# Performance work log

Measured on AMD Instinct MI355X. Metric: run time of the kernel, lower is better.

Reference implementation:

```python
import jax, jax.numpy as jnp
import numpy as np

N_NODES = 50000
N_EDGES = 800000
MUL = 32      # node feature multiplicity (32x0e)
A = 8         # node attr multiplicity (8x0e)
VE = 4        # edge attr multiplicity (4x0e)
FC_IN = 16    # edge_scalars dim (fc_neurons[0])
FC_H = 64     # fc hidden (fc_neurons[1])
W_NUMEL = MUL * VE  # tp.weight_numel for 'uvu' instruction = 128
NUM_NEIGHBORS = 16
N_LAYERS = 2


def fctp(x, y, w):
    # FullyConnectedTensorProduct on pure scalars: x[n,U], y[n,V], w[U,V,K]
    U, V = w.shape[0], w.shape[1]
    return jnp.einsum('nu,nv,uvk->nk', x, y, w) / np.float32(np.sqrt(U * V))


def tp_uvu(x, y, w):
    # 'uvu' TensorProduct with per-edge weights: x[e,U], y[e,V], w[e,U,V]
    V = y.shape[1]
    return jnp.einsum('eu,ev,euv->eu', x, y, w) / np.float32(np.sqrt(V))


def conv_layer(node_in, node_attr, edge_src, edge_dst, edge_attr, edge_scalars,
               sc_w, lin1_w, lin2_w, alpha_w, sce_w, fc_w0, fc_w1):
    n_nodes = node_in.shape[0]
    # per-edge weight generation (FullyConnectedNet with sin activation)
    h = jnp.sin(edge_scalars @ fc_w0 / np.float32(np.sqrt(FC_IN)))          # [E, FC_H]
    w = (h @ fc_w1 / np.float32(np.sqrt(FC_H))).reshape(-1, MUL, VE)        # [E, MUL, VE]
    # self connection + lin1
    node_sc = fctp(node_in, node_attr, sc_w)                                # [N, K]
    x = fctp(node_in, node_attr, lin1_w)                                    # [N, MUL]
    # gather -> tensor product -> scatter-add
    edge_features = tp_uvu(x[edge_src], edge_attr, w)                       # [E, MUL]
    node_features = jax.ops.segment_sum(edge_features, edge_dst,
                                        num_segments=n_nodes)
    node_features = node_features / np.float32(np.sqrt(NUM_NEIGHBORS))      # [N, MUL]
    node_conv = fctp(node_features, node_attr, lin2_w)                      # [N, K]
    alpha = fctp(node_features, node_attr, alpha_w)                         # [N, 1]
    # output_mask is all ones for scalar outputs -> alpha = 1 - 1 + alpha*1
    node_out = node_sc + alpha * node_conv
    edge_out = edge_attr + fctp(edge_features, edge_attr, sce_w) / np.float32(np.sqrt(NUM_NEIGHBORS))
    return node_out, edge_out


def setup_inputs() -> dict:
    key = jax.random.key(0)
    ks = jax.random.split(key, 13)
    L = N_LAYERS
    return {
        'node_features': jax.random.normal(ks[0], (N_NODES, MUL), jnp.float32),
        'node_attr':     jax.random.normal(ks[1], (N_NODES, A), jnp.float32),
        'edge_src':      jax.random.randint(ks[2], (N_EDGES,), 0, N_NODES),
        'edge_dst':      jax.random.randint(ks[3], (N_EDGES,), 0, N_NODES),
        'edge_attr':     jax.random.normal(ks[4], (N_EDGES, VE), jnp.float32),
        'edge_scalars':  jax.random.normal(ks[5], (N_EDGES, FC_IN), jnp.float32),
        # stacked per-layer parameters
        'sc_w':    jax.random.normal(ks[6],  (L, MUL, A, MUL), jnp.float32),
        'lin1_w':  jax.random.normal(ks[7],  (L, MUL, A, MUL), jnp.float32),
        'lin2_w':  jax.random.normal(ks[8],  (L, MUL, A, MUL), jnp.float32),
        'alpha_w': 0.1 * jax.random.normal(ks[9], (L, MUL, A, 1), jnp.float32),
        'sce_w':   jax.random.normal(ks[10], (L, MUL, VE, VE), jnp.float32),
        'fc_w0':   jax.random.normal(ks[11], (L, FC_IN, FC_H), jnp.float32),
        'fc_w1':   jax.random.normal(ks[12], (L, FC_H, W_NUMEL), jnp.float32),
    }


def reference(node_features, node_attr, edge_src, edge_dst, edge_attr, edge_scalars,
              sc_w, lin1_w, lin2_w, alpha_w, sce_w, fc_w0, fc_w1):
    nf, ea = node_features, edge_attr
    for l in range(N_LAYERS):
        nf, ea = conv_layer(nf, node_attr, edge_src, edge_dst, ea, edge_scalars,
                            sc_w[l], lin1_w[l], lin2_w[l], alpha_w[l],
                            sce_w[l], fc_w0[l], fc_w1[l])
        if l < N_LAYERS - 1:
            nf = jnp.sin(nf)  # Gate over even scalars == elementwise sin
    return nf, ea
```

## Files before the change

kernel.cpp:

```cpp
#include <hip/hip_runtime.h>
#include <hip/hip_bf16.h>


namespace {
constexpr int NN = 50000;
constexpr int NE = 800000;
constexpr int SCAN_BLOCKS = 196;

constexpr long OFF_NF   = 0;
constexpr long OFF_W0P  = 1600000;
constexpr long OFF_W2P  = 1602048;
constexpr long OFF_WNP  = 1610240;
constexpr long OFF_OFF  = 1638912;
constexpr long OFF_CUR  = 1688913;
constexpr long OFF_PERM = 1738913;
constexpr long OFF_BSUM = 2538913;
constexpr long OFF_EF   = 2539172;
}

typedef __attribute__((ext_vector_type(8))) short short8;
typedef __attribute__((ext_vector_type(4))) float f32x4;
typedef unsigned int   __attribute__((may_alias)) u32a;
typedef unsigned short __attribute__((may_alias)) u16a;
typedef float          __attribute__((may_alias)) f32a;

__device__ __forceinline__ float us2f(unsigned int u) {
    unsigned int x = u << 16; float f;
    __builtin_memcpy(&f, &x, sizeof(f));
    return f;
}
__device__ __forceinline__ unsigned short f2us(float f) {
    __hip_bfloat16 h = __float2bfloat16(f);
    unsigned short s;
    __builtin_memcpy(&s, &h, sizeof(s));
    return s;
}

__global__ __launch_bounds__(256) void k_hist(
        const int* __restrict__ dst, int* __restrict__ cnt,
        const float* __restrict__ f0, const float* __restrict__ f1,
        const float* __restrict__ l1w, const float* __restrict__ scw,
        const float* __restrict__ l2w, const float* __restrict__ aw,
        unsigned short* __restrict__ w0p, unsigned short* __restrict__ w2p,
        unsigned short* __restrict__ wnp) {
    int i = blockIdx.x * 256 + threadIdx.x;
    if (i < NE) atomicAdd(&cnt[dst[i]], 1);
    if (i < 4096) {
        int l = i >> 11, r = i & 2047;
        int nt = r >> 9, lane = (r >> 3) & 63, ii = r & 7;
        int k = (lane >> 4) * 8 + ii;
        int j = nt * 16 + (lane & 15);
        float v = (k < 16) ? 0.25f * f0[l * 1024 + k * 64 + j] : 0.f;
        w0p[i] = f2us(v);
    }
    if (i < 16384) {
        int l = i >> 13, r = i & 8191;
        int g = r >> 9;
        int kt = g >> 1, nt = g & 1;
        int lane = (r >> 3) & 63, ii = r & 7;
        int K = kt * 32 + (lane >> 4) * 8 + ii;
        int j = K >> 2, v = K & 3;
        int u = nt * 16 + (lane & 15);
        w2p[i] = f2us(f1[l * 8192 + j * 128 + u * 4 + v]);
    }
    if (i < 57344) {
        int l = i / 28672, r = i % 28672;
        int tile = r >> 12;
        int r2 = r & 4095;
        int kt = r2 >> 9, lane = (r2 >> 3) & 63, ii = r2 & 7;
        int k = kt * 32 + (lane >> 4) * 8 + ii;
        int u = k >> 3, v = k & 7;
        int col = lane & 15;
        int uvb = l * 8192 + (u * 8 + v) * 32;
        float val;
        if (tile < 2)      val = l1w[uvb + tile * 16 + col];
        else if (tile < 4) val = scw[uvb + (tile - 2) * 16 + col];
        else if (tile < 6) val = l2w[uvb + (tile - 4) * 16 + col];
        else               val = (col == 0) ? aw[l * 256 + u * 8 + v] : 0.f;
        wnp[i] = f2us(val);
    }
}

__global__ __launch_bounds__(256) void k_scan1(const int* __restrict__ cnt,
                                               int* __restrict__ bsum) {
    __shared__ int s[256];
    int t = threadIdx.x;
    int i = blockIdx.x * 256 + t;
    s[t] = (i < NN) ? cnt[i] : 0;
    __syncthreads();
    for (int d = 128; d > 0; d >>= 1) {
        if (t < d) s[t] += s[t + d];
        __syncthreads();
    }
    if (t == 0) bsum[blockIdx.x] = s[0];
}

__global__ __launch_bounds__(256) void k_scan2(int* __restrict__ bsum) {
    __shared__ int s[256];
    int t = threadIdx.x;
    int v = (t < SCAN_BLOCKS) ? bsum[t] : 0;
    s[t] = v; __syncthreads();
    for (int d = 1; d < 256; d <<= 1) {
        int x = (t >= d) ? s[t - d] : 0;
        __syncthreads();
        s[t] += x;
        __syncthreads();
    }
    if (t < SCAN_BLOCKS) bsum[t] = s[t] - v;
}

__global__ __launch_bounds__(256) void k_scan3(
        const int* __restrict__ cnt, const int* __restrict__ bsum,
        int* __restrict__ off, int* __restrict__ cur) {
    __shared__ int s[256];
    int t = threadIdx.x;
    int i = blockIdx.x * 256 + t;
    int v = (i < NN) ? cnt[i] : 0;
    s[t] = v; __syncthreads();
    for (int d = 1; d < 256; d <<= 1) {
        int x = (t >= d) ? s[t - d] : 0;
        __syncthreads();
        s[t] += x;
        __syncthreads();
    }
    int excl = s[t] - v + bsum[blockIdx.x];
    if (i < NN) { off[i] = excl; cur[i] = excl; }
    if (i == NN - 1) off[NN] = excl + v;
}

__global__ void k_perm(const int* __restrict__ dst, int* __restrict__ cur,
                       int* __restrict__ perm) {
    int e = blockIdx.x * 256 + threadIdx.x;
    if (e >= NE) return;
    perm[e] = atomicAdd(&cur[dst[e]], 1);
}

__device__ __forceinline__ void stage_xy(const float* __restrict__ nf,
                                         const float* __restrict__ nattr,
                                         long n0, int t, f32a* Xs, f32a* Ys) {
    {
        long e = n0 * 32 + t * 8;
        int n = t >> 2, u = (t & 3) * 8;
        f32a* d = &Xs[n * 33 + u];
        if (e + 8 <= (long)NN * 32) {
            const float4* p = (const float4*)(nf + e);
            float4 q0 = p[0], q1 = p[1];
            d[0]=q0.x; d[1]=q0.y; d[2]=q0.z; d[3]=q0.w;
            d[4]=q1.x; d[5]=q1.y; d[6]=q1.z; d[7]=q1.w;
        } else {
#pragma unroll
            for (int i = 0; i < 8; i++)
                d[i] = (e + i < (long)NN * 32) ? nf[e + i] : 0.f;
        }
    }
    if (t < 128) {
        long e = n0 * 8 + t * 4;
        int n = t >> 1, v = (t & 1) * 4;
        f32a* d = &Ys[n * 9 + v];
        if (e + 4 <= (long)NN * 8) {
            float4 q = *(const float4*)(nattr + e);
            d[0]=q.x; d[1]=q.y; d[2]=q.z; d[3]=q.w;
        } else {
#pragma unroll
            for (int i = 0; i < 4; i++)
                d[i] = (e + i < (long)NN * 8) ? nattr[e + i] : 0.f;
        }
    }
}

__global__ __launch_bounds__(256) void k_npre_m(
        const float* __restrict__ nf, const float* __restrict__ nattr,
        const unsigned short* __restrict__ wnp_l, float* __restrict__ xl) {
    __shared__ f32a Xs[64 * 33];
    __shared__ f32a Ys[64 * 9];
    const int t = threadIdx.x;
    const long n0 = (long)blockIdx.x * 64;
    stage_xy(nf, nattr, n0, t, Xs, Ys);
    __syncthreads();

    const int lane = t & 63, w = t >> 6;
    const int l15 = lane & 15, quad = lane >> 4;
    const int nb = w * 16;
    float y[8], xk[8];
#pragma unroll
    for (int v = 0; v < 8; v++) y[v] = Ys[(nb + l15) * 9 + v];
#pragma unroll
    for (int kt = 0; kt < 8; kt++) xk[kt] = Xs[(nb + l15) * 33 + kt * 4 + quad];

    f32x4 a0, a1;
    a0[0]=0.f;a0[1]=0.f;a0[2]=0.f;a0[3]=0.f;
    a1[0]=0.f;a1[1]=0.f;a1[2]=0.f;a1[3]=0.f;
#pragma unroll
    for (int kt = 0; kt < 8; kt++) {
        float xv = xk[kt];
        short8 a;
#pragma unroll
        for (int i = 0; i < 8; i++) a[i] = (short)f2us(xv * y[i]);
        const short8 b0 = *(const short8*)(wnp_l + ((0 * 8 + kt) * 512) + lane * 8);
        const short8 b1 = *(const short8*)(wnp_l + ((1 * 8 + kt) * 512) + lane * 8);
        a0 = __builtin_amdgcn_mfma_f32_16x16x32_bf16(a, b0, a0, 0, 0, 0);
        a1 = __builtin_amdgcn_mfma_f32_16x16x32_bf16(a, b1, a1, 0, 0, 0);
    }
#pragma unroll
    for (int r = 0; r < 4; r++) {
        long n = n0 + nb + quad * 4 + r;
        if (n < NN) {
            xl[n * 32 + l15]      = a0[r] * 0.0625f;
            xl[n * 32 + 16 + l15] = a1[r] * 0.0625f;
        }
    }
}

__global__ __launch_bounds__(256) void k_edge_w(
        const float* __restrict__ esc, const int* __restrict__ srcp,
        const int* __restrict__ perm, const float* __restrict__ ea_in,
        float* __restrict__ ea_out, const float* __restrict__ xl,
        const unsigned short* __restrict__ w0p,
        const unsigned short* __restrict__ w2p,
        const float* __restrict__ sew, unsigned short* __restrict__ ef_bf) {
    __shared__ __align__(16) unsigned char SCR[4][8704];

    const int t = threadIdx.x;
    const int w = t >> 6, lane = t & 63;
    const int l15 = lane & 15, quad = lane >> 4;
    const long e0 = ((long)blockIdx.x * 4 + w) * 64;
    u16a* Hs = (u16a*)SCR[w];
    f32a* Ts = (f32a*)SCR[w];

    short8 bw0[4];
#pragma unroll
    for (int nt = 0; nt < 4; nt++)
        bw0[nt] = *(const short8*)(w0p + (nt * 64 + lane) * 8);
#pragma unroll
    for (int mt = 0; mt < 4; mt++) {
        int row = mt * 16 + l15;
        short8 a;
#pragma unroll
        for (int i = 0; i < 8; i++) a[i] = 0;
        if (quad < 2) {
            const float4* ep = (const float4*)(esc + (e0 + row) * 16 + quad * 8);
            float4 p0 = ep[0], p1 = ep[1];
            a[0]=(short)f2us(p0.x); a[1]=(short)f2us(p0.y);
            a[2]=(short)f2us(p0.z); a[3]=(short)f2us(p0.w);
            a[4]=(short)f2us(p1.x); a[5]=(short)f2us(p1.y);
            a[6]=(short)f2us(p1.z); a[7]=(short)f2us(p1.w);
        }
#pragma unroll
        for (int nt = 0; nt < 4; nt++) {
            f32x4 c; c[0]=0.f; c[1]=0.f; c[2]=0.f; c[3]=0.f;
            c = __builtin_amdgcn_mfma_f32_16x16x32_bf16(a, bw0[nt], c, 0, 0, 0);
#pragma unroll
            for (int r = 0; r < 4; r++) {
                int edge = mt * 16 + quad * 4 + r;
                int j = nt * 16 + l15;
                Hs[edge * 68 + j] = f2us(__sinf(c[r]));
            }
        }
    }
    __syncthreads();

    f32x4 acc[4][2];
#pragma unroll
    for (int mt = 0; mt < 4; mt++)
#pragma unroll
        for (int nt = 0; nt < 2; nt++) {
            acc[mt][nt][0]=0.f; acc[mt][nt][1]=0.f;
            acc[mt][nt][2]=0.f; acc[mt][nt][3]=0.f;
        }
#pragma unroll
    for (int mt = 0; mt < 4; mt++) {
        int row = mt * 16 + l15;
        float4 eaq = ((const float4*)ea_in)[e0 + row];
#pragma unroll
        for (int kt = 0; kt < 8; kt++) {
            unsigned int hp = *(const u32a*)(Hs + row * 68 + kt * 8 + quad * 2);
            float H0 = us2f(hp & 0xFFFFu), H1 = us2f(hp >> 16);
            short8 a;
            a[0]=(short)f2us(H0*eaq.x); a[1]=(short)f2us(H0*eaq.y);
            a[2]=(short)f2us(H0*eaq.z); a[3]=(short)f2us(H0*eaq.w);
            a[4]=(short)f2us(H1*eaq.x); a[5]=(short)f2us(H1*eaq.y);
            a[6]=(short)f2us(H1*eaq.z); a[7]=(short)f2us(H1*eaq.w);
            const short8 b0 = *(const short8*)(w2p + ((kt*2+0)*64 + lane) * 8);
            const short8 b1 = *(const short8*)(w2p + ((kt*2+1)*64 + lane) * 8);
            acc[mt][0] = __builtin_amdgcn_mfma_f32_16x16x32_bf16(a, b0, acc[mt][0], 0, 0, 0);
            acc[mt][1] = __builtin_amdgcn_mfma_f32_16x16x32_bf16(a, b1, acc[mt][1], 0, 0, 0);
        }
    }
    __syncthreads();
#pragma unroll
    for (int mt = 0; mt < 4; mt++)
#pragma unroll
        for (int nt = 0; nt < 2; nt++)
#pragma unroll
            for (int r = 0; r < 4; r++)
                Ts[(mt*16 + quad*4 + r) * 34 + nt*16 + l15] = acc[mt][nt][r] * 0.125f;

    {
        long ge = e0 + lane;
        float tv[32];
#pragma unroll
        for (int u = 0; u < 32; u++) tv[u] = Ts[lane * 34 + u];
        int src = srcp[ge], pm = perm[ge];
        float4 eaq = ((const float4*)ea_in)[ge];
        float ea[4] = {eaq.x, eaq.y, eaq.z, eaq.w};
        const float4* xp = (const float4*)(xl + (long)src * 32);
        float ef[32];
#pragma unroll
        for (int g = 0; g < 8; g++) {
            float4 xq = xp[g];
            ef[4*g+0] = 0.5f * xq.x * tv[4*g+0];
            ef[4*g+1] = 0.5f * xq.y * tv[4*g+1];
            ef[4*g+2] = 0.5f * xq.z * tv[4*g+2];
            ef[4*g+3] = 0.5f * xq.w * tv[4*g+3];
        }
        uint4* efp = (uint4*)(ef_bf + (long)pm * 32);
#pragma unroll
        for (int g = 0; g < 4; g++) {
            uint4 wv;
            wv.x = (unsigned)f2us(ef[8*g+0]) | ((unsigned)f2us(ef[8*g+1]) << 16);
            wv.y = (unsigned)f2us(ef[8*g+2]) | ((unsigned)f2us(ef[8*g+3]) << 16);
            wv.z = (unsigned)f2us(ef[8*g+4]) | ((unsigned)f2us(ef[8*g+5]) << 16);
            wv.w = (unsigned)f2us(ef[8*g+6]) | ((unsigned)f2us(ef[8*g+7]) << 16);
            efp[g] = wv;
        }
        float eo[4] = {0.f, 0.f, 0.f, 0.f};
#pragma unroll
        for (int u = 0; u < 32; u++) {
            float efu = ef[u];
#pragma unroll
            for (int v = 0; v < 4; v++) {
                float p = efu * ea[v];
                const float* sw = sew + (u * 4 + v) * 4;
#pragma unroll
                for (int k = 0; k < 4; k++) eo[k] = fmaf(p, sw[k], eo[k]);
            }
        }
        constexpr float SCE_SCALE = 0.02209708691f;
        float4 o;
        o.x = ea[0] + eo[0]*SCE_SCALE; o.y = ea[1] + eo[1]*SCE_SCALE;
        o.z = ea[2] + eo[2]*SCE_SCALE; o.w = ea[3] + eo[3]*SCE_SCALE;
        ((float4*)ea_out)[ge] = o;
    }
}

__global__ __launch_bounds__(256) void k_gpost_m(
        const int* __restrict__ off, const unsigned short* __restrict__ ef,
        const float* __restrict__ nf_cur, const float* __restrict__ nattr,
        const unsigned short* __restrict__ wnp_l,
        float* __restrict__ nf_next, float* __restrict__ out_nf, int last) {
    __shared__ f32a Xs[64 * 33];
    __shared__ f32a As[64 * 33];
    __shared__ f32a Ys[64 * 9];
    const int t = threadIdx.x;
    const long n0 = (long)blockIdx.x * 64;
    stage_xy(nf_cur, nattr, n0, t, Xs, Ys);

    {
        int slot = t >> 3, g = (t >> 2) & 1, l4 = t & 3;
#pragma unroll
        for (int batch = 0; batch < 2; batch++) {
            int nl = batch * 32 + slot;
            long n = n0 + nl;
            float v[8] = {0.f,0.f,0.f,0.f,0.f,0.f,0.f,0.f};
            if (n < NN) {
                int b = off[n] + g, en = off[n + 1];
                for (int r = b; r < en; r += 2) {
                    uint4 q = *(const uint4*)(ef + (long)r * 32 + l4 * 8);
                    v[0] += us2f(q.x & 0xFFFFu); v[1] += us2f(q.x >> 16);
                    v[2] += us2f(q.y & 0xFFFFu); v[3] += us2f(q.y >> 16);
                    v[4] += us2f(q.z & 0xFFFFu); v[5] += us2f(q.z >> 16);
                    v[6] += us2f(q.w & 0xFFFFu); v[7] += us2f(q.w >> 16);
                }
            }
#pragma unroll
            for (int i = 0; i < 8; i++) v[i] += __shfl_xor(v[i], 4);
            if (g == 0) {
#pragma unroll
                for (int i = 0; i < 8; i++)
                    As[nl * 33 + l4 * 8 + i] = v[i] * 0.25f;
            }
        }
    }
    __syncthreads();

    const int lane = t & 63, w = t >> 6;
    const int l15 = lane & 15, quad = lane >> 4;
    const int nb = w * 16;
    float y[8], xk[8], ak[8];
#pragma unroll
    for (int v = 0; v < 8; v++) y[v] = Ys[(nb + l15) * 9 + v];
#pragma unroll
    for (int kt = 0; kt < 8; kt++) {
        xk[kt] = Xs[(nb + l15) * 33 + kt * 4 + quad];
        ak[kt] = As[(nb + l15) * 33 + kt * 4 + quad];
    }
    f32x4 sc0, sc1, l20, l21, al;
    sc0[0]=0.f;sc0[1]=0.f;sc0[2]=0.f;sc0[3]=0.f;
    sc1 = sc0; l20 = sc0; l21 = sc0; al = sc0;
#pragma unroll
    for (int kt = 0; kt < 8; kt++) {
        float xv = xk[kt], av = ak[kt];
        short8 ax, ag;
#pragma unroll
        for (int i = 0; i < 8; i++) {
            ax[i] = (short)f2us(xv * y[i]);
            ag[i] = (short)f2us(av * y[i]);
        }
        const short8 b2 = *(const short8*)(wnp_l + ((2 * 8 + kt) * 512) + lane * 8);
        const short8 b3 = *(const short8*)(wnp_l + ((3 * 8 + kt) * 512) + lane * 8);
        const short8 b4 = *(const short8*)(wnp_l + ((4 * 8 + kt) * 512) + lane * 8);
        const short8 b5 = *(const short8*)(wnp_l + ((5 * 8 + kt) * 512) + lane * 8);
        const short8 b6 = *(const short8*)(wnp_l + ((6 * 8 + kt) * 512) + lane * 8);
        sc0 = __builtin_amdgcn_mfma_f32_16x16x32_bf16(ax, b2, sc0, 0, 0, 0);
        sc1 = __builtin_amdgcn_mfma_f32_16x16x32_bf16(ax, b3, sc1, 0, 0, 0);
        l20 = __builtin_amdgcn_mfma_f32_16x16x32_bf16(ag, b4, l20, 0, 0, 0);
        l21 = __builtin_amdgcn_mfma_f32_16x16x32_bf16(ag, b5, l21, 0, 0, 0);
        al  = __builtin_amdgcn_mfma_f32_16x16x32_bf16(ag, b6, al,  0, 0, 0);
    }
#pragma unroll
    for (int r = 0; r < 4; r++) {
        float alpha = __shfl(al[r], quad * 16) * 0.0625f;
        long n = n0 + nb + quad * 4 + r;
        if (n < NN) {
            float o0 = sc0[r] * 0.0625f + alpha * (l20[r] * 0.0625f);
            float o1 = sc1[r] * 0.0625f + alpha * (l21[r] * 0.0625f);
            if (last) {
                out_nf[n * 32 + l15]      = o0;
                out_nf[n * 32 + 16 + l15] = o1;
            } else {
                nf_next[n * 32 + l15]      = __sinf(o0);
                nf_next[n * 32 + 16 + l15] = __sinf(o1);
            }
        }
    }
}

extern "C" void kernel_launch(void* const* d_in, const int* in_sizes, int n_in,
                              void* d_out, int out_size, void* d_ws, size_t ws_size,
                              hipStream_t stream) {
    int I_nf, I_na, I_esrc, I_edst, I_ea, I_esc, I_sc, I_l1, I_l2, I_al, I_se, I_f0, I_f1;
    if (in_sizes[0] == 1600000) {
        I_nf=0; I_na=1; I_esrc=2; I_edst=3; I_ea=4; I_esc=5;
        I_sc=6; I_l1=7; I_l2=8; I_al=9; I_se=10; I_f0=11; I_f1=12;
    } else {
        I_al=0; I_ea=1; I_edst=2; I_esc=3; I_esrc=4; I_f0=5; I_f1=6;
        I_l1=7; I_l2=8; I_na=9; I_nf=10; I_sc=11; I_se=12;
    }
    const float* nf_in = (const float*)d_in[I_nf];
    const float* na    = (const float*)d_in[I_na];
    const int*   esrc  = (const int*)d_in[I_esrc];
    const int*   edst  = (const int*)d_in[I_edst];
    const float* ea_in = (const float*)d_in[I_ea];
    const float* escl  = (const float*)d_in[I_esc];
    const float* w_sc  = (const float*)d_in[I_sc];
    const float* w_l1  = (const float*)d_in[I_l1];
    const float* w_l2  = (const float*)d_in[I_l2];
    const float* w_al  = (const float*)d_in[I_al];
    const float* w_se  = (const float*)d_in[I_se];
    const float* w_f0  = (const float*)d_in[I_f0];
    const float* w_f1  = (const float*)d_in[I_f1];

    float* ws = (float*)d_ws;
    float* out_nf = (float*)d_out;
    float* out_ea = out_nf + (long)NN * 32;

    unsigned short* w0p     = (unsigned short*)(ws + OFF_W0P);
    unsigned short* w2p     = (unsigned short*)(ws + OFF_W2P);
    unsigned short* wnp     = (unsigned short*)(ws + OFF_WNP);
    int*            csr_off = (int*)(ws + OFF_OFF);
    int*            csr_cur = (int*)(ws + OFF_CUR);
    int*            perm    = (int*)(ws + OFF_PERM);
    int*            bsum    = (int*)(ws + OFF_BSUM);
    unsigned short* ef_bf   = (unsigned short*)(ws + OFF_EF);

    hipMemsetAsync(csr_cur, 0, NN * sizeof(int), stream);
    k_hist<<<3125, 256, 0, stream>>>(edst, csr_cur, w_f0, w_f1,
                                     w_l1, w_sc, w_l2, w_al, w0p, w2p, wnp);
    k_scan1<<<SCAN_BLOCKS, 256, 0, stream>>>(csr_cur, bsum);
    k_scan2<<<1, 256, 0, stream>>>(bsum);
    k_scan3<<<SCAN_BLOCKS, 256, 0, stream>>>(csr_cur, bsum, csr_off, csr_cur);
    k_perm<<<3125, 256, 0, stream>>>(edst, csr_cur, perm);

    for (int l = 0; l < 2; l++) {
        int last = (l == 1);
        const float* nf_cur = (l == 0) ? nf_in : (ws + OFF_NF);
        const float* ea_cur = (l == 0) ? ea_in : out_ea;

        k_npre_m<<<782, 256, 0, stream>>>(nf_cur, na, wnp + l * 28672,
                                          out_nf );
        k_edge_w<<<3125, 256, 0, stream>>>(escl, esrc, perm, ea_cur, out_ea,
                                           out_nf , w0p + l * 2048,
                                           w2p + l * 8192, w_se + l * 512,
                                           ef_bf);
        k_gpost_m<<<782, 256, 0, stream>>>(csr_off, ef_bf,
                                           nf_cur, na, wnp + l * 28672,
                                           ws + OFF_NF, out_nf, last);
    }
}
```

Baseline: 406.6 us.

## Fuse next-layer lin1 into gather-post kernel and use packed bf16 conversions

Merges the second layer's node pre-transform (lin1) into the first layer's gather/post kernel, so the sin-activated node features are reused from shared memory instead of being re-read by a separate launch. It also replaces scalar float-to-bf16 conversions with a packed two-value conversion builtin where available. The edge weight GEMM loop is reordered so B fragments are loaded once per k-step across all row tiles. The extra kernel phase adds synchronisation and register pressure in the post kernel.

```diff
diff --git a/kernel.cpp b/kernel.cpp
--- a/kernel.cpp
+++ b/kernel.cpp
@@ -34,6 +34,27 @@
     unsigned short s;
     __builtin_memcpy(&s, &h, sizeof(s));
     return s;
+}
+
+#if defined(__has_builtin)
+#  if __has_builtin(__builtin_amdgcn_cvt_pk_bf16_f32)
+#    define PKBF16 1
+#  endif
+#endif
+__device__ __forceinline__ unsigned int f2us2(float a, float b) {
+#ifdef PKBF16
+    auto r = __builtin_amdgcn_cvt_pk_bf16_f32(a, b);
+    unsigned int u; __builtin_memcpy(&u, &r, 4);
+    return u;
+#else
+    return (unsigned)f2us(a) | ((unsigned)f2us(b) << 16);
+#endif
+}
+__device__ __forceinline__ short8 mk_frag(unsigned int u0, unsigned int u1,
+                                          unsigned int u2, unsigned int u3) {
+    unsigned int u[4] = {u0, u1, u2, u3};
+    short8 a; __builtin_memcpy(&a, u, 16);
+    return a;
 }
 
 __global__ __launch_bounds__(256) void k_hist(
@@ -193,9 +214,8 @@
 #pragma unroll
     for (int kt = 0; kt < 8; kt++) {
         float xv = xk[kt];
-        short8 a;
-#pragma unroll
-        for (int i = 0; i < 8; i++) a[i] = (short)f2us(xv * y[i]);
+        short8 a = mk_frag(f2us2(xv*y[0], xv*y[1]), f2us2(xv*y[2], xv*y[3]),
+                           f2us2(xv*y[4], xv*y[5]), f2us2(xv*y[6], xv*y[7]));
         const short8 b0 = *(const short8*)(wnp_l + ((0 * 8 + kt) * 512) + lane * 8);
         const short8 b1 = *(const short8*)(wnp_l + ((1 * 8 + kt) * 512) + lane * 8);
         a0 = __builtin_amdgcn_mfma_f32_16x16x32_bf16(a, b0, a0, 0, 0, 0);
@@ -240,10 +260,8 @@
         if (quad < 2) {
             const float4* ep = (const float4*)(esc + (e0 + row) * 16 + quad * 8);
             float4 p0 = ep[0], p1 = ep[1];
-            a[0]=(short)f2us(p0.x); a[1]=(short)f2us(p0.y);
-            a[2]=(short)f2us(p0.z); a[3]=(short)f2us(p0.w);
-            a[4]=(short)f2us(p1.x); a[5]=(short)f2us(p1.y);
-            a[6]=(short)f2us(p1.z); a[7]=(short)f2us(p1.w);
+            a = mk_frag(f2us2(p0.x, p0.y), f2us2(p0.z, p0.w),
+                        f2us2(p1.x, p1.y), f2us2(p1.z, p1.w));
         }
 #pragma unroll
         for (int nt = 0; nt < 4; nt++) {
@@ -267,21 +285,22 @@
             acc[mt][nt][0]=0.f; acc[mt][nt][1]=0.f;
             acc[mt][nt][2]=0.f; acc[mt][nt][3]=0.f;
         }
-#pragma unroll
-    for (int mt = 0; mt < 4; mt++) {
-        int row = mt * 16 + l15;
-        float4 eaq = ((const float4*)ea_in)[e0 + row];
-#pragma unroll
-        for (int kt = 0; kt < 8; kt++) {
+    float4 eaq_r[4];
+#pragma unroll
+    for (int mt = 0; mt < 4; mt++)
+        eaq_r[mt] = ((const float4*)ea_in)[e0 + mt * 16 + l15];
+#pragma unroll
+    for (int kt = 0; kt < 8; kt++) {
+        const short8 b0 = *(const short8*)(w2p + ((kt*2+0)*64 + lane) * 8);
+        const short8 b1 = *(const short8*)(w2p + ((kt*2+1)*64 + lane) * 8);
+#pragma unroll
+        for (int mt = 0; mt < 4; mt++) {
+            int row = mt * 16 + l15;
             unsigned int hp = *(const u32a*)(Hs + row * 68 + kt * 8 + quad * 2);
             float H0 = us2f(hp & 0xFFFFu), H1 = us2f(hp >> 16);
-            short8 a;
-            a[0]=(short)f2us(H0*eaq.x); a[1]=(short)f2us(H0*eaq.y);
-            a[2]=(short)f2us(H0*eaq.z); a[3]=(short)f2us(H0*eaq.w);
-            a[4]=(short)f2us(H1*eaq.x); a[5]=(short)f2us(H1*eaq.y);
-            a[6]=(short)f2us(H1*eaq.z); a[7]=(short)f2us(H1*eaq.w);
-            const short8 b0 = *(const short8*)(w2p + ((kt*2+0)*64 + lane) * 8);
-            const short8 b1 = *(const short8*)(w2p + ((kt*2+1)*64 + lane) * 8);
+            float4 ea = eaq_r[mt];
+            short8 a = mk_frag(f2us2(H0*ea.x, H0*ea.y), f2us2(H0*ea.z, H0*ea.w),
+                               f2us2(H1*ea.x, H1*ea.y), f2us2(H1*ea.z, H1*ea.w));
             acc[mt][0] = __builtin_amdgcn_mfma_f32_16x16x32_bf16(a, b0, acc[mt][0], 0, 0, 0);
             acc[mt][1] = __builtin_amdgcn_mfma_f32_16x16x32_bf16(a, b1, acc[mt][1], 0, 0, 0);
         }
@@ -317,10 +336,10 @@
 #pragma unroll
         for (int g = 0; g < 4; g++) {
             uint4 wv;
-            wv.x = (unsigned)f2us(ef[8*g+0]) | ((unsigned)f2us(ef[8*g+1]) << 16);
-            wv.y = (unsigned)f2us(ef[8*g+2]) | ((unsigned)f2us(ef[8*g+3]) << 16);
-            wv.z = (unsigned)f2us(ef[8*g+4]) | ((unsigned)f2us(ef[8*g+5]) << 16);
-            wv.w = (unsigned)f2us(ef[8*g+6]) | ((unsigned)f2us(ef[8*g+7]) << 16);
+            wv.x = f2us2(ef[8*g+0], ef[8*g+1]);
+            wv.y = f2us2(ef[8*g+2], ef[8*g+3]);
+            wv.z = f2us2(ef[8*g+4], ef[8*g+5]);
+            wv.w = f2us2(ef[8*g+6], ef[8*g+7]);
             efp[g] = wv;
         }
         float eo[4] = {0.f, 0.f, 0.f, 0.f};
@@ -343,11 +362,13 @@
     }
 }
 
-__global__ __launch_bounds__(256) void k_gpost_m(
+__global__ __launch_bounds__(256) void k_gpost_f(
         const int* __restrict__ off, const unsigned short* __restrict__ ef,
         const float* __restrict__ nf_cur, const float* __restrict__ nattr,
         const unsigned short* __restrict__ wnp_l,
-        float* __restrict__ nf_next, float* __restrict__ out_nf, int last) {
+        const unsigned short* __restrict__ wnp_nx,
+        float* __restrict__ nf_next, float* __restrict__ out_nf,
+        float* __restrict__ xl, int last) {
     __shared__ f32a Xs[64 * 33];
     __shared__ f32a As[64 * 33];
     __shared__ f32a Ys[64 * 9];
@@ -400,12 +421,10 @@
 #pragma unroll
     for (int kt = 0; kt < 8; kt++) {
         float xv = xk[kt], av = ak[kt];
-        short8 ax, ag;
-#pragma unroll
-        for (int i = 0; i < 8; i++) {
-            ax[i] = (short)f2us(xv * y[i]);
-            ag[i] = (short)f2us(av * y[i]);
-        }
+        short8 ax = mk_frag(f2us2(xv*y[0], xv*y[1]), f2us2(xv*y[2], xv*y[3]),
+                            f2us2(xv*y[4], xv*y[5]), f2us2(xv*y[6], xv*y[7]));
+        short8 ag = mk_frag(f2us2(av*y[0], av*y[1]), f2us2(av*y[2], av*y[3]),
+                            f2us2(av*y[4], av*y[5]), f2us2(av*y[6], av*y[7]));
         const short8 b2 = *(const short8*)(wnp_l + ((2 * 8 + kt) * 512) + lane * 8);
         const short8 b3 = *(const short8*)(wnp_l + ((3 * 8 + kt) * 512) + lane * 8);
         const short8 b4 = *(const short8*)(wnp_l + ((4 * 8 + kt) * 512) + lane * 8);
@@ -417,20 +436,58 @@
         l21 = __builtin_amdgcn_mfma_f32_16x16x32_bf16(ag, b5, l21, 0, 0, 0);
         al  = __builtin_amdgcn_mfma_f32_16x16x32_bf16(ag, b6, al,  0, 0, 0);
     }
+    float s0v[4], s1v[4];
 #pragma unroll
     for (int r = 0; r < 4; r++) {
         float alpha = __shfl(al[r], quad * 16) * 0.0625f;
         long n = n0 + nb + quad * 4 + r;
-        if (n < NN) {
-            float o0 = sc0[r] * 0.0625f + alpha * (l20[r] * 0.0625f);
-            float o1 = sc1[r] * 0.0625f + alpha * (l21[r] * 0.0625f);
-            if (last) {
+        float o0 = sc0[r] * 0.0625f + alpha * (l20[r] * 0.0625f);
+        float o1 = sc1[r] * 0.0625f + alpha * (l21[r] * 0.0625f);
+        if (last) {
+            if (n < NN) {
                 out_nf[n * 32 + l15]      = o0;
                 out_nf[n * 32 + 16 + l15] = o1;
-            } else {
-                nf_next[n * 32 + l15]      = __sinf(o0);
-                nf_next[n * 32 + 16 + l15] = __sinf(o1);
             }
+        } else {
+            float v0 = __sinf(o0), v1 = __sinf(o1);
+            s0v[r] = v0; s1v[r] = v1;
+            if (n < NN) {
+                nf_next[n * 32 + l15]      = v0;
+                nf_next[n * 32 + 16 + l15] = v1;
+            }
+        }
+    }
+    if (last) return;
+
+    __syncthreads();
+#pragma unroll
+    for (int r = 0; r < 4; r++) {
+        Xs[(nb + quad * 4 + r) * 33 + l15]      = s0v[r];
+        Xs[(nb + quad * 4 + r) * 33 + 16 + l15] = s1v[r];
+    }
+    __syncthreads();
+    float xk2[8];
+#pragma unroll
+    for (int kt = 0; kt < 8; kt++) xk2[kt] = Xs[(nb + l15) * 33 + kt * 4 + quad];
+    f32x4 a0, a1;
+    a0[0]=0.f;a0[1]=0.f;a0[2]=0.f;a0[3]=0.f;
+    a1 = a0;
+#pragma unroll
+    for (int kt = 0; kt < 8; kt++) {
+        float xv = xk2[kt];
+        short8 a = mk_frag(f2us2(xv*y[0], xv*y[1]), f2us2(xv*y[2], xv*y[3]),
+                           f2us2(xv*y[4], xv*y[5]), f2us2(xv*y[6], xv*y[7]));
+        const short8 b0 = *(const short8*)(wnp_nx + ((0 * 8 + kt) * 512) + lane * 8);
+        const short8 b1 = *(const short8*)(wnp_nx + ((1 * 8 + kt) * 512) + lane * 8);
+        a0 = __builtin_amdgcn_mfma_f32_16x16x32_bf16(a, b0, a0, 0, 0, 0);
+        a1 = __builtin_amdgcn_mfma_f32_16x16x32_bf16(a, b1, a1, 0, 0, 0);
+    }
+#pragma unroll
+    for (int r = 0; r < 4; r++) {
+        long n = n0 + nb + quad * 4 + r;
+        if (n < NN) {
+            xl[n * 32 + l15]      = a0[r] * 0.0625f;
+            xl[n * 32 + 16 + l15] = a1[r] * 0.0625f;
         }
     }
 }
@@ -481,19 +538,19 @@
     k_scan3<<<SCAN_BLOCKS, 256, 0, stream>>>(csr_cur, bsum, csr_off, csr_cur);
     k_perm<<<3125, 256, 0, stream>>>(edst, csr_cur, perm);
 
-    for (int l = 0; l < 2; l++) {
-        int last = (l == 1);
-        const float* nf_cur = (l == 0) ? nf_in : (ws + OFF_NF);
-        const float* ea_cur = (l == 0) ? ea_in : out_ea;
-
-        k_npre_m<<<782, 256, 0, stream>>>(nf_cur, na, wnp + l * 28672,
-                                          out_nf );
-        k_edge_w<<<3125, 256, 0, stream>>>(escl, esrc, perm, ea_cur, out_ea,
-                                           out_nf , w0p + l * 2048,
-                                           w2p + l * 8192, w_se + l * 512,
-                                           ef_bf);
-        k_gpost_m<<<782, 256, 0, stream>>>(csr_off, ef_bf,
-                                           nf_cur, na, wnp + l * 28672,
-                                           ws + OFF_NF, out_nf, last);
-    }
-}
+    k_npre_m<<<782, 256, 0, stream>>>(nf_in, na, wnp, out_nf );
+
+    k_edge_w<<<3125, 256, 0, stream>>>(escl, esrc, perm, ea_in, out_ea,
+                                       out_nf , w0p, w2p, w_se, ef_bf);
+    k_gpost_f<<<782, 256, 0, stream>>>(csr_off, ef_bf, nf_in, na,
+                                       wnp, wnp + 28672,
+                                       ws + OFF_NF , out_nf,
+                                       out_nf , 0);
+    k_edge_w<<<3125, 256, 0, stream>>>(escl, esrc, perm, out_ea, out_ea,
+                                       out_nf , w0p + 2048,
+                                       w2p + 8192, w_se + 512, ef_bf);
+    k_gpost_f<<<782, 256, 0, stream>>>(csr_off, ef_bf, ws + OFF_NF, na,
+                                       wnp + 28672, wnp ,
+                                       ws + OFF_NF , out_nf,
+                                       out_nf , 1);
+}
```

Result: no change. 410.4 us (+0.9%).
